# Performance work log

Hardware: AMD Instinct MI355X
Metric: run time of the kernel (lower is better)

## Reference

```python
import jax, jax.numpy as jnp
import numpy as np

PI = 3.14159265358979323846
MARGIN = 6.0
DIM = 256
ENT_TOT = 43234
REL_RANGE = (6.0 + 2.0) / DIM  # (margin + epsilon) / dim = 0.03125


def setup_inputs() -> dict:
    key = jax.random.key(0)
    k1, k2, k3 = jax.random.split(key, 3)
    head = jax.random.normal(k1, (32, 2 * DIM), dtype=jnp.float32)
    relation = jax.random.normal(k2, (32, DIM), dtype=jnp.float32)
    ent_emb = jax.random.normal(k3, (ENT_TOT, 2 * DIM), dtype=jnp.float32)
    return {"head": head, "relation": relation, "ent_emb": ent_emb}


def reference(head, relation, ent_emb):
    # head: (B, 2D) -> re/im halves (B, D)
    re_h, im_h = jnp.split(head, 2, axis=-1)
    # entity table: (E, 2D) -> (E, D) each
    re_t, im_t = jnp.split(ent_emb, 2, axis=-1)
    # phase rotation from relation embedding
    phase = relation / (REL_RANGE / PI)          # (B, D)
    re_r = jnp.cos(phase)
    im_r = jnp.sin(phase)
    # complex rotation of head by relation: (B, D)
    re_rot = re_h * re_r - im_h * im_r
    im_rot = re_h * im_r + im_h * re_r
    # difference against every entity, broadcast to (B, E, D)
    re_s = re_rot[:, None, :] - re_t[None, :, :]
    im_s = im_rot[:, None, :] - im_t[None, :, :]
    # L2 norm over the complex pair, summed over D -> (B, E)
    dist = jnp.sqrt(re_s * re_s + im_s * im_s).sum(axis=-1)
    return MARGIN - dist
```

## Files before the change

### kernel.cpp

```cpp
#include <hip/hip_runtime.h>
#include <math.h>

#define DIMH 256
#define NB   32
#define E_TOT 43234
#define TE   32
#define DK   16
#define NCW  4

typedef float v2f __attribute__((ext_vector_type(2)));
typedef float v4f __attribute__((ext_vector_type(4)));
typedef __fp16 v2h __attribute__((ext_vector_type(2)));
typedef __fp16 v4h __attribute__((ext_vector_type(4)));

__global__ __launch_bounds__(64) void rot_kernel(const float* __restrict__ head,
                                                 const float* __restrict__ rel,
                                                 float4* __restrict__ rot_v4) {
    int i  = blockIdx.x * 64 + threadIdx.x;
    int b  = i >> 7;
    int dp = i & 127;
    int d0 = dp * 2;
    float4 w;
    {
        float re_h = head[b * 2 * DIMH + d0];
        float im_h = head[b * 2 * DIMH + DIMH + d0];
        float x = rel[b * DIMH + d0] * 16.0f;
        float f = x - floorf(x);
        float s = __builtin_amdgcn_sinf(f);
        float c = __builtin_amdgcn_cosf(f);
        w.x = re_h * c - im_h * s;
        w.z = re_h * s + im_h * c;
    }
    {
        float re_h = head[b * 2 * DIMH + d0 + 1];
        float im_h = head[b * 2 * DIMH + DIMH + d0 + 1];
        float x = rel[b * DIMH + d0 + 1] * 16.0f;
        float f = x - floorf(x);
        float s = __builtin_amdgcn_sinf(f);
        float c = __builtin_amdgcn_cosf(f);
        w.y = re_h * c - im_h * s;
        w.w = re_h * s + im_h * c;
    }
    rot_v4[b * (DIMH / 2) + dp] = w;
}

__device__ __forceinline__ v2h pkrtz(float a, float b) {
    return __builtin_amdgcn_cvt_pkrtz(a, b);
}

__global__ __launch_bounds__(256) void dist_kernel(const float* __restrict__ ent,
                                                   const float4* __restrict__ rot_v4,
                                                   float* __restrict__ out) {
    __shared__ v4h smem[2176];

    const int tid  = threadIdx.x;
    const int lane = tid & 63;
    const int w    = tid >> 6;
    const int eb   = blockIdx.x * TE;
    const int eg   = lane & 7;
    const int bg   = lane >> 3;

    v4h* se = smem + w * 512;
    v4h* sr = se + 256;

    const int erow = lane >> 2;
    const int eq   = lane & 3;
    const int rb   = lane >> 3;
    const int rdpi = lane & 7;

    const int c0 = w * NCW;

    float4 pe_re[2], pe_im[2], pr[4];

    auto load_chunk = [&](int c) {
        const int dk = c * DK;
        #pragma unroll
        for (int s = 0; s < 2; ++s) {
            int er = min(eb + erow + 16 * s, E_TOT - 1);
            const float* b0 = ent + (size_t)er * (2 * DIMH);
            pe_re[s] = *reinterpret_cast<const float4*>(b0 + dk + 4 * eq);
            pe_im[s] = *reinterpret_cast<const float4*>(b0 + DIMH + dk + 4 * eq);
        }
        #pragma unroll
        for (int s = 0; s < 4; ++s)
            pr[s] = rot_v4[(rb + 8 * s) * (DIMH / 2) + c * (DK / 2) + rdpi];
    };

    auto store_chunk = [&]() {
        #pragma unroll
        for (int s = 0; s < 2; ++s) {
            int row = erow + 16 * s;
            int sw  = row >> 2;
            v4h lo, hi;
            lo.xy = pkrtz(pe_re[s].x, pe_re[s].y);
            lo.zw = pkrtz(pe_im[s].x, pe_im[s].y);
            hi.xy = pkrtz(pe_re[s].z, pe_re[s].w);
            hi.zw = pkrtz(pe_im[s].z, pe_im[s].w);
            se[row * 8 + ((2 * eq)     ^ sw)] = lo;
            se[row * 8 + ((2 * eq + 1) ^ sw)] = hi;
        }
        #pragma unroll
        for (int s = 0; s < 4; ++s) {
            int b  = rb + 8 * s;
            int sw = b >> 2;
            v4h r;
            r.xy = pkrtz(pr[s].x, pr[s].y);
            r.zw = pkrtz(pr[s].z, pr[s].w);
            sr[b * 8 + (rdpi ^ sw)] = r;
        }
    };

    v2f acc[4][4];
    #pragma unroll
    for (int j = 0; j < 4; ++j)
        #pragma unroll
        for (int k = 0; k < 4; ++k) { acc[j][k].x = 0.f; acc[j][k].y = 0.f; }

    load_chunk(c0);

    #pragma unroll 1
    for (int cc = 0; cc < NCW; ++cc) {
        store_chunk();
        if (cc + 1 < NCW) load_chunk(c0 + cc + 1);

        v2h a16[4][4];
        #pragma unroll
        for (int j = 0; j < 4; ++j)
            #pragma unroll
            for (int k = 0; k < 4; ++k) { a16[j][k].x = (__fp16)0.f; a16[j][k].y = (__fp16)0.f; }

        #pragma unroll 4
        for (int p = 0; p < DK / 2; ++p) {
            int pe = p ^ eg, pb = p ^ bg;
            v4h r0 = sr[(4 * bg + 0) * 8 + pb];
            v4h r1 = sr[(4 * bg + 1) * 8 + pb];
            v4h r2 = sr[(4 * bg + 2) * 8 + pb];
            v4h r3 = sr[(4 * bg + 3) * 8 + pb];
            v4h e0 = se[(4 * eg + 0) * 8 + pe];
            v4h e1 = se[(4 * eg + 1) * 8 + pe];
            v4h e2 = se[(4 * eg + 2) * 8 + pe];
            v4h e3 = se[(4 * eg + 3) * 8 + pe];
            #define CONTRIB(J, K, R, E)                              \
                { v2h a = R.xy - E.xy;                               \
                  v2h b = R.zw - E.zw;                               \
                  v2h s = a * a + b * b;                             \
                  a16[J][K] += __builtin_elementwise_sqrt(s); }
            CONTRIB(0,0,r0,e0) CONTRIB(0,1,r0,e1) CONTRIB(0,2,r0,e2) CONTRIB(0,3,r0,e3)
            CONTRIB(1,0,r1,e0) CONTRIB(1,1,r1,e1) CONTRIB(1,2,r1,e2) CONTRIB(1,3,r1,e3)
            CONTRIB(2,0,r2,e0) CONTRIB(2,1,r2,e1) CONTRIB(2,2,r2,e2) CONTRIB(2,3,r2,e3)
            CONTRIB(3,0,r3,e0) CONTRIB(3,1,r3,e1) CONTRIB(3,2,r3,e2) CONTRIB(3,3,r3,e3)
            #undef CONTRIB
        }

        #pragma unroll
        for (int j = 0; j < 4; ++j)
            #pragma unroll
            for (int k = 0; k < 4; ++k) {
                acc[j][k].x += (float)a16[j][k].x;
                acc[j][k].y += (float)a16[j][k].y;
            }
    }

    float part[16];
    #pragma unroll
    for (int j = 0; j < 4; ++j)
        #pragma unroll
        for (int k = 0; k < 4; ++k)
            part[j * 4 + k] = acc[j][k].x + acc[j][k].y;

    __syncthreads();
    float* red = (float*)smem;
    #pragma unroll
    for (int i = 0; i < 16; ++i)
        red[tid * 17 + i] = part[i];
    __syncthreads();

    #pragma unroll
    for (int t = 0; t < 4; ++t) {
        int O  = tid + 256 * t;
        int b  = O >> 5;
        int ei = O & 31;
        int e  = eb + ei;
        if (e < E_TOT) {
            int lane_src = ((b >> 2) << 3) + (ei >> 2);
            int idx      = ((b & 3) << 2) + (ei & 3);
            float sum = red[(0 * 64 + lane_src) * 17 + idx]
                      + red[(1 * 64 + lane_src) * 17 + idx]
                      + red[(2 * 64 + lane_src) * 17 + idx]
                      + red[(3 * 64 + lane_src) * 17 + idx];
            out[(size_t)b * E_TOT + e] = 6.0f - sum;
        }
    }
}

extern "C" void kernel_launch(void* const* d_in, const int* in_sizes, int n_in,
                              void* d_out, int out_size, void* d_ws, size_t ws_size,
                              hipStream_t stream) {
    const float* head = (const float*)d_in[0];
    const float* rel  = (const float*)d_in[1];
    const float* ent  = (const float*)d_in[2];
    float4* rot_v4 = (float4*)d_ws;

    rot_kernel<<<(NB * DIMH / 2) / 64, 64, 0, stream>>>(head, rel, rot_v4);

    int etiles = (E_TOT + TE - 1) / TE;
    dist_kernel<<<etiles, 256, 0, stream>>>(ent, rot_v4, (float*)d_out);
}
```

Before: 177.1 us.

## Halve entity tile per block to launch more blocks and cut register use

Reduces the entity tile per block from 32 to 16. Each thread now computes a 4x2 block of batch-by-entity outputs instead of 4x4, and the shared-memory layout, swizzle and reduction are resized to match. The aim is to double the grid size, lower per-thread register and LDS pressure, and raise occupancy. In exchange, the rotated-relation tile is reloaded from memory twice as often and each relation value loaded from LDS is reused across fewer entities.

Result: faster. 169.7 us (-4.2%).

```diff
diff --git a/kernel.cpp b/kernel.cpp
--- a/kernel.cpp
+++ b/kernel.cpp
@@ -4,7 +4,7 @@
 #define DIMH 256
 #define NB   32
 #define E_TOT 43234
-#define TE   32
+#define TE   16
 #define DK   16
 #define NCW  4
 
@@ -51,7 +51,7 @@
 __global__ __launch_bounds__(256) void dist_kernel(const float* __restrict__ ent,
                                                    const float4* __restrict__ rot_v4,
                                                    float* __restrict__ out) {
-    __shared__ v4h smem[2176];
+    __shared__ v4h smem[1536];
 
     const int tid  = threadIdx.x;
     const int lane = tid & 63;
@@ -60,8 +60,8 @@
     const int eg   = lane & 7;
     const int bg   = lane >> 3;
 
-    v4h* se = smem + w * 512;
-    v4h* sr = se + 256;
+    v4h* se = smem + w * 384;
+    v4h* sr = se + 128;
 
     const int erow = lane >> 2;
     const int eq   = lane & 3;
@@ -70,39 +70,35 @@
 
     const int c0 = w * NCW;
 
-    float4 pe_re[2], pe_im[2], pr[4];
+    float4 pe_re, pe_im, pr[4];
 
     auto load_chunk = [&](int c) {
         const int dk = c * DK;
-        #pragma unroll
-        for (int s = 0; s < 2; ++s) {
-            int er = min(eb + erow + 16 * s, E_TOT - 1);
-            const float* b0 = ent + (size_t)er * (2 * DIMH);
-            pe_re[s] = *reinterpret_cast<const float4*>(b0 + dk + 4 * eq);
-            pe_im[s] = *reinterpret_cast<const float4*>(b0 + DIMH + dk + 4 * eq);
-        }
+        int er = min(eb + erow, E_TOT - 1);
+        const float* b0 = ent + (size_t)er * (2 * DIMH);
+        pe_re = *reinterpret_cast<const float4*>(b0 + dk + 4 * eq);
+        pe_im = *reinterpret_cast<const float4*>(b0 + DIMH + dk + 4 * eq);
         #pragma unroll
         for (int s = 0; s < 4; ++s)
             pr[s] = rot_v4[(rb + 8 * s) * (DIMH / 2) + c * (DK / 2) + rdpi];
     };
 
     auto store_chunk = [&]() {
-        #pragma unroll
-        for (int s = 0; s < 2; ++s) {
-            int row = erow + 16 * s;
-            int sw  = row >> 2;
+        {
+            int row = erow;
+            int sw  = (row >> 1) & 7;
             v4h lo, hi;
-            lo.xy = pkrtz(pe_re[s].x, pe_re[s].y);
-            lo.zw = pkrtz(pe_im[s].x, pe_im[s].y);
-            hi.xy = pkrtz(pe_re[s].z, pe_re[s].w);
-            hi.zw = pkrtz(pe_im[s].z, pe_im[s].w);
+            lo.xy = pkrtz(pe_re.x, pe_re.y);
+            lo.zw = pkrtz(pe_im.x, pe_im.y);
+            hi.xy = pkrtz(pe_re.z, pe_re.w);
+            hi.zw = pkrtz(pe_im.z, pe_im.w);
             se[row * 8 + ((2 * eq)     ^ sw)] = lo;
             se[row * 8 + ((2 * eq + 1) ^ sw)] = hi;
         }
         #pragma unroll
         for (int s = 0; s < 4; ++s) {
             int b  = rb + 8 * s;
-            int sw = b >> 2;
+            int sw = (b >> 2) & 7;
             v4h r;
             r.xy = pkrtz(pr[s].x, pr[s].y);
             r.zw = pkrtz(pr[s].z, pr[s].w);
@@ -110,11 +106,11 @@
         }
     };
 
-    v2f acc[4][4];
+    v2f acc[4][2];
     #pragma unroll
     for (int j = 0; j < 4; ++j)
         #pragma unroll
-        for (int k = 0; k < 4; ++k) { acc[j][k].x = 0.f; acc[j][k].y = 0.f; }
+        for (int k = 0; k < 2; ++k) { acc[j][k].x = 0.f; acc[j][k].y = 0.f; }
 
     load_chunk(c0);
 
@@ -123,11 +119,11 @@
         store_chunk();
         if (cc + 1 < NCW) load_chunk(c0 + cc + 1);
 
-        v2h a16[4][4];
+        v2h a16[4][2];
         #pragma unroll
         for (int j = 0; j < 4; ++j)
             #pragma unroll
-            for (int k = 0; k < 4; ++k) { a16[j][k].x = (__fp16)0.f; a16[j][k].y = (__fp16)0.f; }
+            for (int k = 0; k < 2; ++k) { a16[j][k].x = (__fp16)0.f; a16[j][k].y = (__fp16)0.f; }
 
         #pragma unroll 4
         for (int p = 0; p < DK / 2; ++p) {
@@ -136,58 +132,56 @@
             v4h r1 = sr[(4 * bg + 1) * 8 + pb];
             v4h r2 = sr[(4 * bg + 2) * 8 + pb];
             v4h r3 = sr[(4 * bg + 3) * 8 + pb];
-            v4h e0 = se[(4 * eg + 0) * 8 + pe];
-            v4h e1 = se[(4 * eg + 1) * 8 + pe];
-            v4h e2 = se[(4 * eg + 2) * 8 + pe];
-            v4h e3 = se[(4 * eg + 3) * 8 + pe];
+            v4h e0 = se[(2 * eg + 0) * 8 + pe];
+            v4h e1 = se[(2 * eg + 1) * 8 + pe];
             #define CONTRIB(J, K, R, E)                              \
                 { v2h a = R.xy - E.xy;                               \
                   v2h b = R.zw - E.zw;                               \
                   v2h s = a * a + b * b;                             \
                   a16[J][K] += __builtin_elementwise_sqrt(s); }
-            CONTRIB(0,0,r0,e0) CONTRIB(0,1,r0,e1) CONTRIB(0,2,r0,e2) CONTRIB(0,3,r0,e3)
-            CONTRIB(1,0,r1,e0) CONTRIB(1,1,r1,e1) CONTRIB(1,2,r1,e2) CONTRIB(1,3,r1,e3)
-            CONTRIB(2,0,r2,e0) CONTRIB(2,1,r2,e1) CONTRIB(2,2,r2,e2) CONTRIB(2,3,r2,e3)
-            CONTRIB(3,0,r3,e0) CONTRIB(3,1,r3,e1) CONTRIB(3,2,r3,e2) CONTRIB(3,3,r3,e3)
+            CONTRIB(0,0,r0,e0) CONTRIB(0,1,r0,e1)
+            CONTRIB(1,0,r1,e0) CONTRIB(1,1,r1,e1)
+            CONTRIB(2,0,r2,e0) CONTRIB(2,1,r2,e1)
+            CONTRIB(3,0,r3,e0) CONTRIB(3,1,r3,e1)
             #undef CONTRIB
         }
 
         #pragma unroll
         for (int j = 0; j < 4; ++j)
             #pragma unroll
-            for (int k = 0; k < 4; ++k) {
+            for (int k = 0; k < 2; ++k) {
                 acc[j][k].x += (float)a16[j][k].x;
                 acc[j][k].y += (float)a16[j][k].y;
             }
     }
 
-    float part[16];
+    float part[8];
     #pragma unroll
     for (int j = 0; j < 4; ++j)
         #pragma unroll
-        for (int k = 0; k < 4; ++k)
-            part[j * 4 + k] = acc[j][k].x + acc[j][k].y;
+        for (int k = 0; k < 2; ++k)
+            part[j * 2 + k] = acc[j][k].x + acc[j][k].y;
 
     __syncthreads();
     float* red = (float*)smem;
     #pragma unroll
-    for (int i = 0; i < 16; ++i)
-        red[tid * 17 + i] = part[i];
+    for (int i = 0; i < 8; ++i)
+        red[tid * 9 + i] = part[i];
     __syncthreads();
 
     #pragma unroll
-    for (int t = 0; t < 4; ++t) {
+    for (int t = 0; t < 2; ++t) {
         int O  = tid + 256 * t;
-        int b  = O >> 5;
-        int ei = O & 31;
+        int b  = O >> 4;
+        int ei = O & 15;
         int e  = eb + ei;
         if (e < E_TOT) {
-            int lane_src = ((b >> 2) << 3) + (ei >> 2);
-            int idx      = ((b & 3) << 2) + (ei & 3);
-            float sum = red[(0 * 64 + lane_src) * 17 + idx]
-                      + red[(1 * 64 + lane_src) * 17 + idx]
-                      + red[(2 * 64 + lane_src) * 17 + idx]
-                      + red[(3 * 64 + lane_src) * 17 + idx];
+            int lane_src = ((b >> 2) << 3) + (ei >> 1);
+            int idx      = ((b & 3) << 1) + (ei & 1);
+            float sum = red[(0 * 64 + lane_src) * 9 + idx]
+                      + red[(1 * 64 + lane_src) * 9 + idx]
+                      + red[(2 * 64 + lane_src) * 9 + idx]
+                      + red[(3 * 64 + lane_src) * 9 + idx];
             out[(size_t)b * E_TOT + e] = 6.0f - sum;
         }
     }
```
